# Performance work log

Hardware: AMD Instinct MI355X
Metric: run time of the kernel (lower is better)

## Reference

```python
import jax, jax.numpy as jnp
import numpy as np

NUM_CLASSES = 64
BASE_MARGIN = 0.1
ADAPTIVE_WEIGHT = 0.1
STAT_WEIGHT = 0.1


def setup_inputs() -> dict:
    key = jax.random.key(0)
    k1, k2 = jax.random.split(key)
    feats = jax.random.normal(k1, (4096, 512), dtype=jnp.float32)
    labels = jax.random.randint(k2, (4096,), 0, NUM_CLASSES, dtype=jnp.int64)
    return {"feats": feats, "labels": labels}


def _forward(feats, labels):
    N, D = feats.shape
    # pairwise euclidean distances (torch.cdist p=2), nan-safe sqrt
    sq = jnp.sum(feats * feats, axis=-1)                      # [N]
    d2 = sq[:, None] + sq[None, :] - 2.0 * (feats @ feats.T)  # [N,N]
    d2 = jnp.maximum(d2, 0.0)
    dist = jnp.sqrt(jnp.where(d2 > 0.0, d2, 1.0))
    dist = jnp.where(d2 > 0.0, dist, 0.0)

    # class stats (first-call EMA == batch stats), under stop_gradient (torch.no_grad)
    sg = jax.lax.stop_gradient(feats)
    counts = jax.ops.segment_sum(jnp.ones((N,), feats.dtype), labels, NUM_CLASSES)  # [C]
    denom = jnp.maximum(counts, 1.0)[:, None]
    cmean = jax.ops.segment_sum(sg, labels, NUM_CLASSES) / denom                    # [C,D]
    cmsq = jax.ops.segment_sum(sg * sg, labels, NUM_CLASSES) / denom                # [C,D]
    cvar = jnp.maximum(cmsq - cmean * cmean, 0.0)  # biased variance (unbiased=False)

    # statistical margin per sample: ||f_i - mean[y_i]|| * mean(var[y_i])
    diff = feats - cmean[labels]                               # grads flow via feats only
    center_dist2 = jnp.sum(diff * diff, axis=-1)
    center_dist = jnp.sqrt(jnp.where(center_dist2 > 0.0, center_dist2, 1.0))
    center_dist = jnp.where(center_dist2 > 0.0, center_dist, 0.0)
    uncertainty = jnp.mean(cvar, axis=-1)[labels]              # [N]
    stat_margin = center_dist * uncertainty

    same = labels[:, None] == labels[None, :]                  # [N,N]
    eye = jnp.eye(N, dtype=bool)
    pos_mask = same & ~eye                                     # matches pos_dist > 0 filter
    neg_mask = ~same

    big = jnp.asarray(1e30, dist.dtype)
    hardest_pos = jnp.max(jnp.where(pos_mask, dist, -big), axis=1)
    hardest_neg = jnp.min(jnp.where(neg_mask, dist, big), axis=1)
    pos_cnt = jnp.sum(pos_mask, axis=1).astype(dist.dtype)
    neg_cnt = jnp.sum(neg_mask, axis=1).astype(dist.dtype)
    mean_pos = jnp.sum(jnp.where(pos_mask, dist, 0.0), axis=1) / jnp.maximum(pos_cnt, 1.0)
    mean_neg = jnp.sum(jnp.where(neg_mask, dist, 0.0), axis=1) / jnp.maximum(neg_cnt, 1.0)

    final_margin = (BASE_MARGIN + ADAPTIVE_WEIGHT * (mean_neg - mean_pos)
                    + STAT_WEIGHT * stat_margin)
    per_sample = jax.nn.relu(hardest_pos - hardest_neg + final_margin)

    valid = (pos_cnt > 0) & (neg_cnt > 0)
    n_valid = jnp.sum(valid.astype(dist.dtype))
    loss = jnp.sum(jnp.where(valid, per_sample, 0.0)) / jnp.maximum(n_valid, 1.0)
    return jnp.where(n_valid > 0, loss, 0.0)


def reference(feats, labels):
    return _forward(feats, labels)
```

## Files before the change

### kernel.cpp

```cpp
#include <hip/hip_runtime.h>
#include <hip/hip_bf16.h>


#define NN 4096
#define DD 512
#define NCLS 64

typedef __bf16 bf16x8 __attribute__((ext_vector_type(8)));
typedef float f32x4 __attribute__((ext_vector_type(4)));

__device__ __forceinline__ void gload_lds16(const void* g, void* l) {
  __builtin_amdgcn_global_load_lds(
      (const __attribute__((address_space(1))) void*)g,
      (__attribute__((address_space(3))) void*)l, 16, 0, 0);
}

__global__ __launch_bounds__(512) void k_stats(
    const float* __restrict__ feats, const int* __restrict__ labels,
    float* __restrict__ counts, float* __restrict__ cmean,
    float* __restrict__ uncert) {
  __shared__ __align__(16) int slab[NN];
  __shared__ int list[NN];
  __shared__ int chunk_off[64];
  __shared__ int sM;
  __shared__ float sred[512];
  const int c = blockIdx.x;
  const int t = threadIdx.x;
  const int lane = t & 63;
  const int wv = t >> 6;
  for (int i = t; i < NN; i += 512) slab[i] = labels[i];
  __syncthreads();
  for (int ch = wv; ch < 64; ch += 8) {
    const unsigned long long m = __ballot(slab[ch * 64 + lane] == c);
    if (lane == 0) chunk_off[ch] = __popcll(m);
  }
  __syncthreads();
  if (wv == 0) {
    const int v = chunk_off[lane];
    int inc = v;
#pragma unroll
    for (int off = 1; off < 64; off <<= 1) {
      const int o = __shfl_up(inc, off);
      if (lane >= off) inc += o;
    }
    chunk_off[lane] = inc - v;
    if (lane == 63) sM = inc;
  }
  __syncthreads();
  const int M = sM;
  for (int ch = wv; ch < 64; ch += 8) {
    const bool my = (slab[ch * 64 + lane] == c);
    const unsigned long long m = __ballot(my);
    if (my) {
      const int pos = chunk_off[ch] + __popcll(m & ((1ULL << lane) - 1ULL));
      list[pos] = ch * 64 + lane;
    }
  }
  __syncthreads();
  float s1 = 0.f, s2 = 0.f;
  int m = 0;
  for (; m + 8 <= M; m += 8) {
    float v[8];
#pragma unroll
    for (int e = 0; e < 8; ++e) v[e] = feats[(size_t)list[m + e] * DD + t];
#pragma unroll
    for (int e = 0; e < 8; ++e) { s1 += v[e]; s2 += v[e] * v[e]; }
  }
  for (; m < M; ++m) {
    const float v = feats[(size_t)list[m] * DD + t];
    s1 += v; s2 += v * v;
  }
  const float den = fmaxf((float)M, 1.f);
  const float mean = s1 / den;
  const float var = fmaxf(s2 / den - mean * mean, 0.f);
  cmean[c * DD + t] = mean;
  sred[t] = var;
  __syncthreads();
  for (int s = 256; s > 0; s >>= 1) {
    if (t < s) sred[t] += sred[t + s];
    __syncthreads();
  }
  if (t == 0) {
    uncert[c] = sred[0] / (float)DD;
    counts[c] = (float)M;
  }
}

__global__ __launch_bounds__(256) void k_row(
    const float* __restrict__ feats, const int* __restrict__ labels,
    const float* __restrict__ cmean, unsigned short* __restrict__ fb,
    float* __restrict__ sqb, float* __restrict__ cd2) {
  const int w = threadIdx.x >> 6;
  const int lane = threadIdx.x & 63;
  const int row = blockIdx.x * 4 + w;
  const int lab = labels[row];
  const float4* fr = (const float4*)(feats + (size_t)row * DD);
  const float4* cm = (const float4*)(cmean + (size_t)lab * DD);
  float sq = 0.f, c2 = 0.f;
  unsigned int ob[4];
#pragma unroll
  for (int h = 0; h < 2; ++h) {
    const float4 f = fr[lane * 2 + h];
    const float4 cv = cm[lane * 2 + h];
    const float fe[4] = {f.x, f.y, f.z, f.w};
    const float ce[4] = {cv.x, cv.y, cv.z, cv.w};
    unsigned short us[4];
#pragma unroll
    for (int e = 0; e < 4; ++e) {
      const __bf16 b = (__bf16)fe[e];
      const float bf = (float)b;
      sq += bf * bf;
      const float dd = fe[e] - ce[e];
      c2 += dd * dd;
      us[e] = __builtin_bit_cast(unsigned short, b);
    }
    ob[h * 2]     = (unsigned int)us[0] | ((unsigned int)us[1] << 16);
    ob[h * 2 + 1] = (unsigned int)us[2] | ((unsigned int)us[3] << 16);
  }
  *(uint4*)(fb + (size_t)row * DD + lane * 8) = make_uint4(ob[0], ob[1], ob[2], ob[3]);
#pragma unroll
  for (int off = 32; off > 0; off >>= 1) {
    sq += __shfl_xor(sq, off);
    c2 += __shfl_xor(c2, off);
  }
  if (lane == 0) {
    sqb[row] = sq;
    cd2[row] = c2;
  }
}

__global__ __launch_bounds__(256) void k_gemm(
    const unsigned short* __restrict__ fb, const float* __restrict__ sqb,
    const int* __restrict__ labels,
    float* __restrict__ php, float* __restrict__ phn,
    float* __restrict__ pst, float* __restrict__ pss) {
  __shared__ __align__(16) unsigned short sA[2][128 * 64];
  __shared__ __align__(16) unsigned short sB[2][128 * 64];
  __shared__ int s_labi[128], s_labj[128];
  __shared__ float s_sqi[128], s_sqj[128];

  const int bid = blockIdx.x;
  const int swz = ((bid & 7) << 7) + (bid >> 3);
  const int ib = swz >> 5, jb = swz & 31;
  const int ibase = ib << 7, jbase = jb << 7;
  const int t = threadIdx.x;
  const int lane = t & 63;
  const int w = t >> 6;
  const int wm = w >> 1, wn = w & 1;

  if (t < 128) {
    s_labi[t] = labels[ibase + t];
    s_labj[t] = labels[jbase + t];
    s_sqi[t] = sqb[ibase + t];
    s_sqj[t] = sqb[jbase + t];
  }

  f32x4 acc[4][4];
#pragma unroll
  for (int mi = 0; mi < 4; ++mi)
#pragma unroll
    for (int nj = 0; nj < 4; ++nj)
      acc[mi][nj] = (f32x4){0.f, 0.f, 0.f, 0.f};

  auto stage = [&](int nb, int kt) {
#pragma unroll
    for (int r = 0; r < 4; ++r) {
      const int q = (r << 8) + t;
      const int row = q >> 3;
      const int ch = q & 7;
      const int ksrc = (kt << 6) + ((ch ^ (row & 7)) << 3);
      gload_lds16(fb + (size_t)(ibase + row) * DD + ksrc, &sA[nb][q << 3]);
      gload_lds16(fb + (size_t)(jbase + row) * DD + ksrc, &sB[nb][q << 3]);
    }
  };

  stage(0, 0);
  __syncthreads();

  const int rin = lane & 15;
  const int g4 = lane >> 4;
  const int swzbyte = (g4 ^ (rin & 7)) << 4;
  const int abase = ((wm << 6) + rin) << 7;
  const int bbase = ((wn << 6) + rin) << 7;

  int cur = 0;
  for (int kt = 0; kt < 8; ++kt) {
    if (kt < 7) stage(cur ^ 1, kt + 1);
    const char* A = (const char*)sA[cur];
    const char* B = (const char*)sB[cur];
#pragma unroll
    for (int ks = 0; ks < 2; ++ks) {
      bf16x8 af[4], bg[4];
#pragma unroll
      for (int mi = 0; mi < 4; ++mi)
        af[mi] = *(const bf16x8*)(A + abase + (mi << 11) + (swzbyte ^ (ks << 6)));
#pragma unroll
      for (int nj = 0; nj < 4; ++nj)
        bg[nj] = *(const bf16x8*)(B + bbase + (nj << 11) + (swzbyte ^ (ks << 6)));
#pragma unroll
      for (int mi = 0; mi < 4; ++mi)
#pragma unroll
        for (int nj = 0; nj < 4; ++nj)
          acc[mi][nj] = __builtin_amdgcn_mfma_f32_16x16x32_bf16(
              af[mi], bg[nj], acc[mi][nj], 0, 0, 0);
    }
    __syncthreads();
    cur ^= 1;
  }

  float qj[4];
  int lj[4];
#pragma unroll
  for (int nj = 0; nj < 4; ++nj) {
    const int cl = (wn << 6) + (nj << 4) + rin;
    qj[nj] = s_sqj[cl];
    lj[nj] = s_labj[cl];
  }
  const int jidx = (jb << 1) + wn;
#pragma unroll
  for (int mi = 0; mi < 4; ++mi) {
#pragma unroll
    for (int r = 0; r < 4; ++r) {
      const int rl = (wm << 6) + (mi << 4) + (g4 << 2) + r;
      const float qi = s_sqi[rl];
      const int li = s_labi[rl];
      float hp = 0.f, hn = 1e30f, st = 0.f, ss = 0.f;
#pragma unroll
      for (int nj = 0; nj < 4; ++nj) {
        const float g = acc[mi][nj][r];
        float d2 = qi + qj[nj] - 2.f * g;
        d2 = fmaxf(d2, 0.f);
        const float dist = sqrtf(d2);
        const bool same = (li == lj[nj]);
        const float dp = same ? dist : 0.f;
        hp = fmaxf(hp, dp);
        hn = fminf(hn, same ? 1e30f : dist);
        st += dist;
        ss += dp;
      }
#pragma unroll
      for (int off = 1; off < 16; off <<= 1) {
        hp = fmaxf(hp, __shfl_xor(hp, off));
        hn = fminf(hn, __shfl_xor(hn, off));
        st += __shfl_xor(st, off);
        ss += __shfl_xor(ss, off);
      }
      if (rin == 0) {
        const int grow = ibase + rl;
        php[jidx * NN + grow] = hp;
        phn[jidx * NN + grow] = hn;
        pst[jidx * NN + grow] = st;
        pss[jidx * NN + grow] = ss;
      }
    }
  }
}

__global__ __launch_bounds__(128) void k_fin1(
    const int* __restrict__ labels, const float* __restrict__ counts,
    const float* __restrict__ uncert, const float* __restrict__ cd2,
    const float* __restrict__ php, const float* __restrict__ phn,
    const float* __restrict__ pst, const float* __restrict__ pss,
    float* __restrict__ pf) {
  const int t = threadIdx.x;
  const int row = blockIdx.x * 128 + t;
  float hp = 0.f, hn = 1e30f, st = 0.f, ss = 0.f;
#pragma unroll 8
  for (int j = 0; j < 64; ++j) {
    hp = fmaxf(hp, php[j * NN + row]);
    hn = fminf(hn, phn[j * NN + row]);
    st += pst[j * NN + row];
    ss += pss[j * NN + row];
  }
  const int lab = labels[row];
  const float cnt = counts[lab];
  const float pos = cnt - 1.f;
  const float neg = (float)NN - cnt;
  const float mean_pos = ss / fmaxf(pos, 1.f);
  const float mean_neg = (st - ss) / fmaxf(neg, 1.f);
  const float c2 = cd2[row];
  const float cdist = (c2 > 0.f) ? sqrtf(c2) : 0.f;
  const float margin = 0.1f + 0.1f * (mean_neg - mean_pos) + 0.1f * (cdist * uncert[lab]);
  const float ps = fmaxf(hp - hn + margin, 0.f);
  const bool valid = (pos > 0.f) && (neg > 0.f);
  __shared__ float r1[128], r2[128];
  r1[t] = valid ? ps : 0.f;
  r2[t] = valid ? 1.f : 0.f;
  __syncthreads();
  for (int s = 64; s > 0; s >>= 1) {
    if (t < s) { r1[t] += r1[t + s]; r2[t] += r2[t + s]; }
    __syncthreads();
  }
  if (t == 0) {
    pf[2 * blockIdx.x] = r1[0];
    pf[2 * blockIdx.x + 1] = r2[0];
  }
}

__global__ __launch_bounds__(64) void k_fin2(const float* __restrict__ pf,
                                             float* __restrict__ out) {
  const int t = threadIdx.x;
  float s = 0.f, c = 0.f;
  if (t < 32) { s = pf[2 * t]; c = pf[2 * t + 1]; }
#pragma unroll
  for (int off = 32; off > 0; off >>= 1) {
    s += __shfl_xor(s, off);
    c += __shfl_xor(c, off);
  }
  if (t == 0) out[0] = (c > 0.f) ? (s / fmaxf(c, 1.f)) : 0.f;
}

extern "C" void kernel_launch(void* const* d_in, const int* in_sizes, int n_in,
                              void* d_out, int out_size, void* d_ws, size_t ws_size,
                              hipStream_t stream) {
  (void)in_sizes; (void)n_in; (void)out_size; (void)ws_size;
  const float* feats = (const float*)d_in[0];
  const int* labels = (const int*)d_in[1];
  char* w = (char*)d_ws;
  float* counts = (float*)(w + 0);
  float* uncert = (float*)(w + 1024);
  float* sqb    = (float*)(w + 2048);
  float* cd2    = (float*)(w + 18432);
  float* pf     = (float*)(w + 34816);
  float* cmean  = (float*)(w + 36864);
  unsigned short* fb = (unsigned short*)(w + 167936);
  float* php = (float*)(w + 4362240);
  float* phn = (float*)(w + 5410816);
  float* pst = (float*)(w + 6459392);
  float* pss = (float*)(w + 7507968);

  k_stats<<<dim3(64), dim3(512), 0, stream>>>(feats, labels, counts, cmean, uncert);
  k_row<<<dim3(1024), dim3(256), 0, stream>>>(feats, labels, cmean, fb, sqb, cd2);
  k_gemm<<<dim3(1024), dim3(256), 0, stream>>>(fb, sqb, labels, php, phn, pst, pss);
  k_fin1<<<dim3(32), dim3(128), 0, stream>>>(labels, counts, uncert, cd2,
                                             php, phn, pst, pss, pf);
  k_fin2<<<dim3(1), dim3(64), 0, stream>>>(pf, (float*)d_out);
}
```

Before: 64.68 us.

## Exploit symmetry of distance matrix to compute only upper-triangular tiles

The GEMM grid now covers only the upper-triangular 128x128 tile pairs (528 blocks instead of 1024). Each off-diagonal tile also emits column-wise partial reductions (max/min/sums) for the transposed rows, so the symmetric half of the distance matrix is never recomputed. The main loop also replaces __syncthreads with explicit vmcnt/lgkmcnt waits and raw barriers so the next stage's loads can stay in flight during compute. The cost is extra registers and cross-lane shuffles in the epilogue, a serial loop to decode tile indices, and fewer blocks to spread over the GPU.

```diff
diff --git a/kernel.cpp b/kernel.cpp
--- a/kernel.cpp
+++ b/kernel.cpp
@@ -140,8 +140,10 @@
   __shared__ float s_sqi[128], s_sqj[128];
 
   const int bid = blockIdx.x;
-  const int swz = ((bid & 7) << 7) + (bid >> 3);
-  const int ib = swz >> 5, jb = swz & 31;
+  const int swz = (bid & 7) * 66 + (bid >> 3);
+  int kk = swz, ib = 0;
+  while (kk >= 32 - ib) { kk -= 32 - ib; ++ib; }
+  const int jb = ib + kk;
   const int ibase = ib << 7, jbase = jb << 7;
   const int t = threadIdx.x;
   const int lane = t & 63;
@@ -175,7 +177,6 @@
   };
 
   stage(0, 0);
-  __syncthreads();
 
   const int rin = lane & 15;
   const int g4 = lane >> 4;
@@ -183,9 +184,16 @@
   const int abase = ((wm << 6) + rin) << 7;
   const int bbase = ((wn << 6) + rin) << 7;
 
-  int cur = 0;
+#pragma unroll
   for (int kt = 0; kt < 8; ++kt) {
-    if (kt < 7) stage(cur ^ 1, kt + 1);
+    const int cur = kt & 1;
+    if (kt < 7) {
+      stage(cur ^ 1, kt + 1);
+      asm volatile("s_waitcnt vmcnt(8)" ::: "memory");
+    } else {
+      asm volatile("s_waitcnt vmcnt(0)" ::: "memory");
+    }
+    __builtin_amdgcn_s_barrier();
     const char* A = (const char*)sA[cur];
     const char* B = (const char*)sB[cur];
 #pragma unroll
@@ -204,8 +212,8 @@
           acc[mi][nj] = __builtin_amdgcn_mfma_f32_16x16x32_bf16(
               af[mi], bg[nj], acc[mi][nj], 0, 0, 0);
     }
-    __syncthreads();
-    cur ^= 1;
+    asm volatile("s_waitcnt lgkmcnt(0)" ::: "memory");
+    __builtin_amdgcn_s_barrier();
   }
 
   float qj[4];
@@ -216,6 +224,10 @@
     qj[nj] = s_sqj[cl];
     lj[nj] = s_labj[cl];
   }
+  float hp2[4], hn2[4], st2[4], ss2[4];
+#pragma unroll
+  for (int nj = 0; nj < 4; ++nj) { hp2[nj] = 0.f; hn2[nj] = 1e30f; st2[nj] = 0.f; ss2[nj] = 0.f; }
+
   const int jidx = (jb << 1) + wn;
 #pragma unroll
   for (int mi = 0; mi < 4; ++mi) {
@@ -233,10 +245,15 @@
         const float dist = sqrtf(d2);
         const bool same = (li == lj[nj]);
         const float dp = same ? dist : 0.f;
+        const float dn = same ? 1e30f : dist;
         hp = fmaxf(hp, dp);
-        hn = fminf(hn, same ? 1e30f : dist);
+        hn = fminf(hn, dn);
         st += dist;
         ss += dp;
+        hp2[nj] = fmaxf(hp2[nj], dp);
+        hn2[nj] = fminf(hn2[nj], dn);
+        st2[nj] += dist;
+        ss2[nj] += dp;
       }
 #pragma unroll
       for (int off = 1; off < 16; off <<= 1) {
@@ -251,6 +268,28 @@
         phn[jidx * NN + grow] = hn;
         pst[jidx * NN + grow] = st;
         pss[jidx * NN + grow] = ss;
+      }
+    }
+  }
+
+  if (ib != jb) {
+    const int iidx = (ib << 1) + wm;
+#pragma unroll
+    for (int nj = 0; nj < 4; ++nj) {
+      float hp = hp2[nj], hn = hn2[nj], st = st2[nj], ss = ss2[nj];
+#pragma unroll
+      for (int off = 16; off < 64; off <<= 1) {
+        hp = fmaxf(hp, __shfl_xor(hp, off));
+        hn = fminf(hn, __shfl_xor(hn, off));
+        st += __shfl_xor(st, off);
+        ss += __shfl_xor(ss, off);
+      }
+      if (g4 == 0) {
+        const int grow = jbase + (wn << 6) + (nj << 4) + rin;
+        php[iidx * NN + grow] = hp;
+        phn[iidx * NN + grow] = hn;
+        pst[iidx * NN + grow] = st;
+        pss[iidx * NN + grow] = ss;
       }
     }
   }
@@ -331,7 +370,7 @@
 
   k_stats<<<dim3(64), dim3(512), 0, stream>>>(feats, labels, counts, cmean, uncert);
   k_row<<<dim3(1024), dim3(256), 0, stream>>>(feats, labels, cmean, fb, sqb, cd2);
-  k_gemm<<<dim3(1024), dim3(256), 0, stream>>>(fb, sqb, labels, php, phn, pst, pss);
+  k_gemm<<<dim3(528), dim3(256), 0, stream>>>(fb, sqb, labels, php, phn, pst, pss);
   k_fin1<<<dim3(32), dim3(128), 0, stream>>>(labels, counts, uncert, cd2,
                                              php, phn, pst, pss, pf);
   k_fin2<<<dim3(1), dim3(64), 0, stream>>>(pf, (float*)d_out);
```

New measurement: 72.68 us. 12.4% more time.

## Single-buffer GEMM LDS tiles for higher occupancy and shuffle-reduce finalizer

Applied to the files above, without the earlier changes.

The GEMM kernel drops double-buffered LDS staging in favor of a single buffer with load/sync/compute/sync per k-tile, halving LDS use, and adds a min-blocks hint of 3 so more workgroups fit per CU. Other resident blocks are meant to hide the memory latency that the prefetch pipeline used to cover. The finalizer now uses 256-thread blocks with wavefront shuffle reductions instead of an LDS tree, and the final kernel reduces 16 partials. The risk is exposed load latency within each block and register pressure from the occupancy hint.

```diff
diff --git a/kernel.cpp b/kernel.cpp
--- a/kernel.cpp
+++ b/kernel.cpp
@@ -129,13 +129,13 @@
   }
 }
 
-__global__ __launch_bounds__(256) void k_gemm(
+__global__ __launch_bounds__(256, 3) void k_gemm(
     const unsigned short* __restrict__ fb, const float* __restrict__ sqb,
     const int* __restrict__ labels,
     float* __restrict__ php, float* __restrict__ phn,
     float* __restrict__ pst, float* __restrict__ pss) {
-  __shared__ __align__(16) unsigned short sA[2][128 * 64];
-  __shared__ __align__(16) unsigned short sB[2][128 * 64];
+  __shared__ __align__(16) unsigned short sA[128 * 64];
+  __shared__ __align__(16) unsigned short sB[128 * 64];
   __shared__ int s_labi[128], s_labj[128];
   __shared__ float s_sqi[128], s_sqj[128];
 
@@ -147,6 +147,11 @@
   const int lane = t & 63;
   const int w = t >> 6;
   const int wm = w >> 1, wn = w & 1;
+  const int rin = lane & 15;
+  const int g4 = lane >> 4;
+  const int swzbyte = (g4 ^ (rin & 7)) << 4;
+  const int abase = ((wm << 6) + rin) << 7;
+  const int bbase = ((wn << 6) + rin) << 7;
 
   if (t < 128) {
     s_labi[t] = labels[ibase + t];
@@ -162,32 +167,19 @@
     for (int nj = 0; nj < 4; ++nj)
       acc[mi][nj] = (f32x4){0.f, 0.f, 0.f, 0.f};
 
-  auto stage = [&](int nb, int kt) {
+  for (int kt = 0; kt < 8; ++kt) {
 #pragma unroll
     for (int r = 0; r < 4; ++r) {
       const int q = (r << 8) + t;
       const int row = q >> 3;
       const int ch = q & 7;
       const int ksrc = (kt << 6) + ((ch ^ (row & 7)) << 3);
-      gload_lds16(fb + (size_t)(ibase + row) * DD + ksrc, &sA[nb][q << 3]);
-      gload_lds16(fb + (size_t)(jbase + row) * DD + ksrc, &sB[nb][q << 3]);
-    }
-  };
-
-  stage(0, 0);
-  __syncthreads();
-
-  const int rin = lane & 15;
-  const int g4 = lane >> 4;
-  const int swzbyte = (g4 ^ (rin & 7)) << 4;
-  const int abase = ((wm << 6) + rin) << 7;
-  const int bbase = ((wn << 6) + rin) << 7;
-
-  int cur = 0;
-  for (int kt = 0; kt < 8; ++kt) {
-    if (kt < 7) stage(cur ^ 1, kt + 1);
-    const char* A = (const char*)sA[cur];
-    const char* B = (const char*)sB[cur];
+      gload_lds16(fb + (size_t)(ibase + row) * DD + ksrc, &sA[q << 3]);
+      gload_lds16(fb + (size_t)(jbase + row) * DD + ksrc, &sB[q << 3]);
+    }
+    __syncthreads();
+    const char* A = (const char*)sA;
+    const char* B = (const char*)sB;
 #pragma unroll
     for (int ks = 0; ks < 2; ++ks) {
       bf16x8 af[4], bg[4];
@@ -205,7 +197,6 @@
               af[mi], bg[nj], acc[mi][nj], 0, 0, 0);
     }
     __syncthreads();
-    cur ^= 1;
   }
 
   float qj[4];
@@ -256,14 +247,14 @@
   }
 }
 
-__global__ __launch_bounds__(128) void k_fin1(
+__global__ __launch_bounds__(256) void k_fin1(
     const int* __restrict__ labels, const float* __restrict__ counts,
     const float* __restrict__ uncert, const float* __restrict__ cd2,
     const float* __restrict__ php, const float* __restrict__ phn,
     const float* __restrict__ pst, const float* __restrict__ pss,
     float* __restrict__ pf) {
   const int t = threadIdx.x;
-  const int row = blockIdx.x * 128 + t;
+  const int row = blockIdx.x * 256 + t;
   float hp = 0.f, hn = 1e30f, st = 0.f, ss = 0.f;
 #pragma unroll 8
   for (int j = 0; j < 64; ++j) {
@@ -283,17 +274,21 @@
   const float margin = 0.1f + 0.1f * (mean_neg - mean_pos) + 0.1f * (cdist * uncert[lab]);
   const float ps = fmaxf(hp - hn + margin, 0.f);
   const bool valid = (pos > 0.f) && (neg > 0.f);
-  __shared__ float r1[128], r2[128];
-  r1[t] = valid ? ps : 0.f;
-  r2[t] = valid ? 1.f : 0.f;
-  __syncthreads();
-  for (int s = 64; s > 0; s >>= 1) {
-    if (t < s) { r1[t] += r1[t + s]; r2[t] += r2[t + s]; }
-    __syncthreads();
-  }
+  float s = valid ? ps : 0.f;
+  float c = valid ? 1.f : 0.f;
+#pragma unroll
+  for (int off = 1; off < 64; off <<= 1) {
+    s += __shfl_xor(s, off);
+    c += __shfl_xor(c, off);
+  }
+  __shared__ float ws1[4], ws2[4];
+  const int lane = t & 63;
+  const int wv = t >> 6;
+  if (lane == 0) { ws1[wv] = s; ws2[wv] = c; }
+  __syncthreads();
   if (t == 0) {
-    pf[2 * blockIdx.x] = r1[0];
-    pf[2 * blockIdx.x + 1] = r2[0];
+    pf[2 * blockIdx.x] = ws1[0] + ws1[1] + ws1[2] + ws1[3];
+    pf[2 * blockIdx.x + 1] = ws2[0] + ws2[1] + ws2[2] + ws2[3];
   }
 }
 
@@ -301,9 +296,9 @@
                                              float* __restrict__ out) {
   const int t = threadIdx.x;
   float s = 0.f, c = 0.f;
-  if (t < 32) { s = pf[2 * t]; c = pf[2 * t + 1]; }
-#pragma unroll
-  for (int off = 32; off > 0; off >>= 1) {
+  if (t < 16) { s = pf[2 * t]; c = pf[2 * t + 1]; }
+#pragma unroll
+  for (int off = 1; off < 16; off <<= 1) {
     s += __shfl_xor(s, off);
     c += __shfl_xor(c, off);
   }
@@ -332,7 +327,7 @@
   k_stats<<<dim3(64), dim3(512), 0, stream>>>(feats, labels, counts, cmean, uncert);
   k_row<<<dim3(1024), dim3(256), 0, stream>>>(feats, labels, cmean, fb, sqb, cd2);
   k_gemm<<<dim3(1024), dim3(256), 0, stream>>>(fb, sqb, labels, php, phn, pst, pss);
-  k_fin1<<<dim3(32), dim3(128), 0, stream>>>(labels, counts, uncert, cd2,
+  k_fin1<<<dim3(16), dim3(256), 0, stream>>>(labels, counts, uncert, cd2,
                                              php, phn, pst, pss, pf);
   k_fin2<<<dim3(1), dim3(64), 0, stream>>>(pf, (float*)d_out);
 }
```

After: 63.22 us. 2.2% less time.
